# Kernel tuning notes

Hardware: AMD Instinct MI355X
Metric: run time of the kernel (lower is better)

The kernel has to match this reference:

```python
import jax, jax.numpy as jnp
import numpy as np
from jax.scipy.linalg import solve_triangular

T, DZ, DX = 4096, 64, 64


def setup_inputs() -> dict:
    key = jax.random.key(0)
    ks = jax.random.split(key, 8)
    observations = jax.random.normal(ks[0], (T, DX), jnp.float32)
    # stable transition matrix (spectral radius < 1)
    A = 0.9 * jnp.eye(DZ, dtype=jnp.float32) + (0.05 / np.sqrt(DZ)) * jax.random.normal(ks[1], (DZ, DZ), jnp.float32)
    b = 0.01 * jax.random.normal(ks[2], (DZ,), jnp.float32)
    qf = jax.random.normal(ks[3], (DZ, DZ), jnp.float32) / np.sqrt(DZ)
    Q = qf @ qf.T + 0.1 * jnp.eye(DZ, dtype=jnp.float32)  # SPD process noise
    H = jax.random.normal(ks[4], (DX, DZ), jnp.float32) / np.sqrt(DZ)
    c = 0.01 * jax.random.normal(ks[5], (DX,), jnp.float32)
    rf = jax.random.normal(ks[6], (DX, DX), jnp.float32) / np.sqrt(DX)
    R = rf @ rf.T + 0.1 * jnp.eye(DX, dtype=jnp.float32)  # SPD observation noise
    prior_mean = jnp.zeros((DZ,), jnp.float32)
    prior_cov = jnp.eye(DZ, dtype=jnp.float32)
    return dict(observations=observations, A=A, b=b, Q=Q, H=H, c=c, R=R,
                prior_mean=prior_mean, prior_cov=prior_cov)


def _update(m, P, y, H, c, R):
    # Kalman update + Gaussian log-likelihood term (stable Cholesky form of
    # the torch.inverse / MultivariateNormal math).
    yhat = H @ m + c                      # predicted obs mean
    S = H @ P @ H.T + R                   # innovation covariance [dx,dx]
    K = jnp.linalg.solve(S, H @ P).T      # gain = P H^T S^{-1} (S, P symmetric)
    r = y - yhat
    fm = m + K @ r
    fP = P - K @ H @ P
    L = jnp.linalg.cholesky(S)
    z = solve_triangular(L, r, lower=True)
    dx = y.shape[0]
    ll = (-0.5 * dx * jnp.log(2.0 * jnp.pi)
          - jnp.sum(jnp.log(jnp.diag(L)))
          - 0.5 * jnp.sum(z * z))
    return fm, fP, ll


def reference(observations, A, b, Q, H, c, R, prior_mean, prior_cov):
    # ---- filter ----
    fm0, fP0, ll0 = _update(prior_mean, prior_cov, observations[0], H, c, R)

    def fstep(carry, y):
        m, P = carry
        pm = A @ m + b                    # predict
        pP = A @ P @ A.T + Q
        fm, fP, ll = _update(pm, pP, y, H, c, R)
        return (fm, fP), (pm, pP, fm, fP, ll)

    _, (pms, pPs, fms, fPs, lls) = jax.lax.scan(fstep, (fm0, fP0), observations[1:])
    pm = jnp.concatenate([prior_mean[None], pms])   # [T, dz]
    pP = jnp.concatenate([prior_cov[None], pPs])    # [T, dz, dz]
    fm = jnp.concatenate([fm0[None], fms])
    fP = jnp.concatenate([fP0[None], fPs])
    loglikelihood = ll0 + jnp.sum(lls)

    # ---- RTS smoother (backward recursion) ----
    def bstep(carry, xs):
        sm, sP = carry
        fmt, fPt, pmn, pPn = xs
        C = jnp.linalg.solve(pPn, A @ fPt).T          # fP A^T pP^{-1}
        sm_t = fmt + C @ (sm - pmn)
        sP_t = fPt + C @ (sP - pPn) @ C.T
        return (sm_t, sP_t), (sm_t, sP_t)

    _, (sms, sPs) = jax.lax.scan(bstep, (fm[-1], fP[-1]),
                                 (fm[:-1], fP[:-1], pm[1:], pP[1:]), reverse=True)
    smoothed_means = jnp.concatenate([sms, fm[-1][None]])
    smoothed_covs = jnp.concatenate([sPs, fP[-1][None]])
    return smoothed_means, smoothed_covs, loglikelihood
```

## Files before the change

kernel.cpp:

```cpp
#include <hip/hip_runtime.h>
#include <math.h>

#define NN 64
#define LDW 68
#define LCH 32
#define N1CAP 144
#define N0MAX 144
#define EPS_HARD 1e-5f
#define EPS_GATE 5e-2f
#define STALL_WIN 5
#define STALL_IMP 0.75f

struct KP {
  const float *Y, *A, *b, *Q, *H, *c, *R, *pm0, *P0;
  float *out_mean, *out_cov, *out_ll;
  int *meta; float *metaF;
  float *fm;
  float *AT, *HT, *HA, *Hb;
  float *Fss, *Kss, *Sinvss, *Css, *CsTss, *pPss, *sPss, *Fpow, *Cpow32, *Cpow31, *uss;
  float *Pw2, *Pw4, *Pw8, *Pw16, *Pw64, *Pw128;
  float *FpwHi, *CpwHi;
  float *Dmss, *dvnss;
  float *scanF0, *scanF1, *scanB0, *scanB1;
  float *ld_pref, *u_pref;
// ... 51 lines not shown
    int base = (e>>6)*LDW + (e&63);
    *(float4*)(D + base) = *(const float4*)(S + base);
  }
  __syncthreads();
}
__device__ __forceinline__ void set_id(float* W) {
  for (int e = threadIdx.x; e < 4096; e += 256)
    W[(e>>6)*LDW + (e&63)] = ((e>>6) == (e&63)) ? 1.f : 0.f;
  __syncthreads();
}
__device__ __forceinline__ void store_id_sub(float* G, const float* W) {
  for (int e = threadIdx.x; e < 4096; e += 256)
    G[e] = (((e>>6) == (e&63)) ? 1.f : 0.f) - W[(e>>6)*LDW + (e&63)];
  __syncthreads();
}
__device__ __forceinline__ void rsub_store(float* Gd, const float* Gs, const float* W) {
  for (int e = threadIdx.x*4; e < 4096; e += 1024) {
    int base = (e>>6)*LDW + (e&63);
    F4 a, g; a.v = *(const float4*)(W + base); g.v = *(const float4*)(Gs + e);
    F4 o; o.f[0]=g.f[0]-a.f[0]; o.f[1]=g.f[1]-a.f[1]; o.f[2]=g.f[2]-a.f[2]; o.f[3]=g.f[3]-a.f[3];
    *(float4*)(Gd + e) = o.v;
  }
  __syncthreads();
}

__device__ __forceinline__ void redpair(float& ma, float& md, float* red) {
  #pragma unroll
  for (int off = 32; off; off >>= 1) {
    ma = fmaxf(ma, __shfl_xor(ma, off, 64));
    md = fmaxf(md, __shfl_xor(md, off, 64));
  }
  const int w = threadIdx.x >> 6;
  if ((threadIdx.x & 63) == 0) { red[w] = ma; red[4 + w] = md; }
  __syncthreads();
  ma = fmaxf(fmaxf(red[0], red[1]), fmaxf(red[2], red[3]));
  md = fmaxf(fmaxf(red[4], red[5]), fmaxf(red[6], red[7]));
  __syncthreads();
}

template<int TRANSA, int TRANSB, int MODE, int LDD>
__device__ __forceinline__ void mm(float* __restrict__ D,
    const float* __restrict__ A, int lda,
    const float* __restrict__ B, int ldb,
    const float* __restrict__ ADD, int ldadd)
{
  const int tid = threadIdx.x;
  const int i0 = (tid >> 4) << 2, j0 = (tid & 15) << 2;
  float acc[4][4] = {};
  for (int k0 = 0; k0 < NN; k0 += 4) {
    F4 av[4], bv[4];
    #pragma unroll
    for (int u = 0; u < 4; ++u) {
      bv[u].v = TRANSB ? *(const float4*)(B + (j0+u)*ldb + k0)
                       : *(const float4*)(B + (k0+u)*ldb + j0);
      av[u].v = TRANSA ? *(const float4*)(A + (k0+u)*lda + i0)
                       : *(const float4*)(A + (i0+u)*lda + k0);
    }
    #pragma unroll
    for (int kk = 0; kk < 4; ++kk) {
      #pragma unroll
      for (int di = 0; di < 4; ++di) {
        float a = TRANSA ? av[kk].f[di] : av[di].f[kk];
        #pragma unroll
        for (int dj = 0; dj < 4; ++dj) {
          float bb = TRANSB ? bv[dj].f[kk] : bv[kk].f[dj];
          acc[di][dj] += a * bb;
        }
      }
    }
  }
  #pragma unroll
  for (int di = 0; di < 4; ++di) {
    if (MODE == 0 && (LDD & 3) == 0) {
      F4 o;
      #pragma unroll
      for (int dj = 0; dj < 4; ++dj) o.f[dj] = acc[di][dj];
      *(float4*)(D + (i0+di)*LDD + j0) = o.v;
    } else {
      #pragma unroll
      for (int dj = 0; dj < 4; ++dj) {
        float v = acc[di][dj];
        if (MODE == 1) v = ADD[(i0+di)*ldadd + j0+dj] + v;
        if (MODE == 2) v = ADD[(i0+di)*ldadd + j0+dj] - v;
        D[(i0+di)*LDD + j0+dj] = v;
      }
    }
  }
  __syncthreads();
}

template<int TA1,int TB1,int MO1,int LD1, int TA2,int TB2,int MO2,int LD2>
__device__ __forceinline__ void mm2(
    float* __restrict__ D1, const float* __restrict__ A1, int lda1,
    const float* __restrict__ B1, int ldb1, const float* __restrict__ AD1, int ldad1,
    float* __restrict__ D2, const float* __restrict__ A2, int lda2,
    const float* __restrict__ B2, int ldb2, const float* __restrict__ AD2, int ldad2)
{
  const int tid = threadIdx.x;
  const int i0 = (tid >> 4) << 2, j0 = (tid & 15) << 2;
  float acc1[4][4] = {}, acc2[4][4] = {};
  for (int k0 = 0; k0 < NN; k0 += 4) {
    F4 av1[4], bv1[4], av2[4], bv2[4];
    #pragma unroll
    for (int u = 0; u < 4; ++u) {
      bv1[u].v = TB1 ? *(const float4*)(B1 + (j0+u)*ldb1 + k0)
                     : *(const float4*)(B1 + (k0+u)*ldb1 + j0);
      av1[u].v = TA1 ? *(const float4*)(A1 + (k0+u)*lda1 + i0)
                     : *(const float4*)(A1 + (i0+u)*lda1 + k0);
      bv2[u].v = TB2 ? *(const float4*)(B2 + (j0+u)*ldb2 + k0)
                     : *(const float4*)(B2 + (k0+u)*ldb2 + j0);
      av2[u].v = TA2 ? *(const float4*)(A2 + (k0+u)*lda2 + i0)
                     : *(const float4*)(A2 + (i0+u)*lda2 + k0);
    }
    #pragma unroll
    for (int kk = 0; kk < 4; ++kk) {
      #pragma unroll
      for (int di = 0; di < 4; ++di) {
        float a1 = TA1 ? av1[kk].f[di] : av1[di].f[kk];
        float a2 = TA2 ? av2[kk].f[di] : av2[di].f[kk];
        #pragma unroll
        for (int dj = 0; dj < 4; ++dj) {
          acc1[di][dj] += a1 * (TB1 ? bv1[dj].f[kk] : bv1[kk].f[dj]);
          acc2[di][dj] += a2 * (TB2 ? bv2[dj].f[kk] : bv2[kk].f[dj]);
        }
      }
    }
  }
  #pragma unroll
  for (int di = 0; di < 4; ++di) {
    if (MO1 == 0 && (LD1 & 3) == 0) {
      F4 o;
      #pragma unroll
      for (int dj = 0; dj < 4; ++dj) o.f[dj] = acc1[di][dj];
      *(float4*)(D1 + (i0+di)*LD1 + j0) = o.v;
    } else {
      #pragma unroll
      for (int dj = 0; dj < 4; ++dj) {
        float v = acc1[di][dj];
        if (MO1 == 1) v = AD1[(i0+di)*ldad1 + j0+dj] + v;
        if (MO1 == 2) v = AD1[(i0+di)*ldad1 + j0+dj] - v;
        D1[(i0+di)*LD1 + j0+dj] = v;
      }
    }
  }
  #pragma unroll
  for (int di = 0; di < 4; ++di) {
    if (MO2 == 0 && (LD2 & 3) == 0) {
      F4 o;
      #pragma unroll
      for (int dj = 0; dj < 4; ++dj) o.f[dj] = acc2[di][dj];
      *(float4*)(D2 + (i0+di)*LD2 + j0) = o.v;
    } else {
      #pragma unroll
      for (int dj = 0; dj < 4; ++dj) {
        float v = acc2[di][dj];
        if (MO2 == 1) v = AD2[(i0+di)*ldad2 + j0+dj] + v;
        if (MO2 == 2) v = AD2[(i0+di)*ldad2 + j0+dj] - v;
        D2[(i0+di)*LD2 + j0+dj] = v;
      }
    }
  }
  __syncthreads();
}

template<bool WANTLOG>
__device__ __forceinline__ void chol68(float* __restrict__ Sm, float* part, float* invd) {
  const int tid = threadIdx.x;
  const int lane = tid & 63;
  #pragma unroll
  for (int p = 0; p < 4; ++p) {
    const int j0 = p * 16;
    if (p > 0) {
      const int i = tid & 63;
      const int jq = (tid >> 6) * 4;
      float acc[4] = {0.f, 0.f, 0.f, 0.f};
      for (int kb = 0; kb < j0; kb += 4) {
        F4 av; av.v = *(const float4*)(Sm + i*LDW + kb);
        #pragma unroll
        for (int q = 0; q < 4; ++q) {
          F4 bv; bv.v = *(const float4*)(Sm + (j0 + jq + q)*LDW + kb);
          acc[q] += av.f[0]*bv.f[0] + av.f[1]*bv.f[1] + av.f[2]*bv.f[2] + av.f[3]*bv.f[3];
        }
      }
      #pragma unroll
      for (int q = 0; q < 4; ++q)
        Sm[i*LDW + j0 + jq + q] -= acc[q];
      __syncthreads();
    }
    if (tid < 64) {
      float t[16];
      F4 tv;
      #pragma unroll
      for (int q4 = 0; q4 < 4; ++q4) {
        tv.v = *(const float4*)(Sm + lane*LDW + j0 + 4*q4);
        t[4*q4] = tv.f[0]; t[4*q4+1] = tv.f[1]; t[4*q4+2] = tv.f[2]; t[4*q4+3] = tv.f[3];
      }
      #pragma unroll
      for (int jj = 0; jj < 16; ++jj) {
        float acc = t[jj];
        #pragma unroll
        for (int kk = 0; kk < jj; ++kk)
          acc -= __shfl(t[kk], j0 + jj, 64) * t[kk];
        float piv = __shfl(acc, j0 + jj, 64);
        float sq = sqrtf(fmaxf(piv, 1e-30f));
        float inv = 1.0f / sq;
        if (lane == j0 + jj) {
          t[jj] = sq;
          invd[j0 + jj] = inv;
          if (WANTLOG) part[j0 + jj] = logf(sq);
        } else {
          t[jj] = (lane > j0 + jj) ? acc * inv : 0.f;
        }
      }
      #pragma unroll
      for (int q4 = 0; q4 < 4; ++q4) {
        tv.f[0] = t[4*q4]; tv.f[1] = t[4*q4+1]; tv.f[2] = t[4*q4+2]; tv.f[3] = t[4*q4+3];
        *(float4*)(Sm + lane*LDW + j0 + 4*q4) = tv.v;
      }
    }
    __syncthreads();
  }
}

template<int TR>
__device__ __forceinline__ void tri_fwd_ld(const float* __restrict__ L,
                                           const float* __restrict__ invd,
                                           const float* __restrict__ SRC, int lds,
                                           float* __restrict__ DST, int ldd) {
  const int col = threadIdx.x >> 2, p = threadIdx.x & 3;
  const int gbase = (threadIdx.x & 63) & ~3;
  float xr[16];
  #pragma unroll
  for (int u = 0; u < 16; ++u)
    xr[u] = TR ? SRC[col*lds + (4*u+p)] : SRC[(4*u+p)*lds + col];
  #pragma unroll
  for (int i = 0; i < NN; ++i) {
    const int idx = i >> 2, ow = i & 3;
    float yi = xr[idx] * invd[i];
    yi = __shfl(yi, gbase + ow, 64);
    if (p == ow) xr[idx] = yi;
    else if (p > ow) xr[idx] -= L[(4*idx+p)*LDW + i] * yi;
    #pragma unroll
// ... 189 lines not shown
    if (p == ow) xr[idx] = yi;
    else if (p < ow) xr[idx] -= L[i*LDW + 4*idx+p] * yi;
    if (p == ow) xs[idx] = zi;
    else if (p < ow) xs[idx] -= L[i*LDW + 4*idx+p] * zi;
    #pragma unroll
    for (int u = 0; u < idx; ++u) {
      xr[u] -= L[i*LDW + 4*u+p] * yi;
      xs[u] -= L[i*LDW + 4*u+p] * zi;
    }
  }
  #pragma unroll
  for (int u = 0; u < 16; ++u) {
    X1[(4*u+p)*LDW + col] = xr[u];
    X2[(4*u+p)*LDW + col] = xs[u];
  }
  __syncthreads();
}

__device__ __forceinline__ void matvec2(float* __restrict__ y,
    const float* __restrict__ M1, const float* __restrict__ x1,
    const float* __restrict__ M2, const float* __restrict__ x2,
    const float* __restrict__ addv, float* __restrict__ red) {
  const int r = threadIdx.x & 63, p = threadIdx.x >> 6;
  const int kb = p*16;
  float s = 0.f;
  #pragma unroll
  for (int q = 0; q < 4; ++q) {
    F4 mv; mv.v = *(const float4*)(M1 + r*NN + kb + q*4);
    s += mv.f[0]*x1[kb+q*4] + mv.f[1]*x1[kb+q*4+1] + mv.f[2]*x1[kb+q*4+2] + mv.f[3]*x1[kb+q*4+3];
    F4 nv; nv.v = *(const float4*)(M2 + r*NN + kb + q*4);
    s += nv.f[0]*x2[kb+q*4] + nv.f[1]*x2[kb+q*4+1] + nv.f[2]*x2[kb+q*4+2] + nv.f[3]*x2[kb+q*4+3];
  }
  red[p*64 + r] = s;
  __syncthreads();
  if (threadIdx.x < 64) {
    float t = red[r] + red[64+r] + red[128+r] + red[192+r];
    y[r] = t + addv[r];
  }
  __syncthreads();
}

__device__ __forceinline__ void matvec256(float* __restrict__ y, const float* __restrict__ Mg,
    const float* __restrict__ x, const float* __restrict__ addv, float* __restrict__ red) {
  const int r = threadIdx.x & 63, p = threadIdx.x >> 6;
  const int kb = p*16;
  float s = 0.f;
  #pragma unroll
  for (int q = 0; q < 4; ++q) {
    F4 mv; mv.v = *(const float4*)(Mg + r*NN + kb + q*4);
    s += mv.f[0]*x[kb+q*4] + mv.f[1]*x[kb+q*4+1] + mv.f[2]*x[kb+q*4+2] + mv.f[3]*x[kb+q*4+3];
  }
  red[p*64 + r] = s;
  __syncthreads();
  if (threadIdx.x < 64) {
    float t = red[r] + red[64+r] + red[128+r] + red[192+r];
    y[r] = t + (addv ? addv[r] : 0.f);
  }
  __syncthreads();
}


__global__ __launch_bounds__(256) void k0(KP P) {
  __shared__ __align__(16) float W0[LDW*NN];
  const int tid = threadIdx.x;
  for (int e = tid; e < 4096; e += 256) {
    int r = e>>6, cc = e&63;
    P.AT[e] = P.A[cc*64+r];
    P.HT[e] = P.H[cc*64+r];
  }
  if (tid < 64) {
    float s = 0.f;
    for (int k = 0; k < 64; ++k) s += P.H[tid*64+k]*P.b[k];
    P.Hb[tid] = s;
  }
  __syncthreads();
  mm<0,0,0,LDW>(W0, P.H, NN, P.A, NN, nullptr, 0);
  l2g(P.HA, W0);
}

__global__ __launch_bounds__(256) void kA(KP P) {
  __shared__ __align__(16) float LA[LDW*NN], LC[LDW*NN], LJ[LDW*NN], LL[LDW*NN];
  __shared__ __align__(16) float W0[LDW*NN], W1[LDW*NN], W2[LDW*NN], W3[LDW*NN], W4[LDW*NN];
  __shared__ float part[64], iv1[64], iv2[64];
  const int tid = threadIdx.x;
  mm2<0,0,0,LDW, 0,0,0,LDW>(W0, P.H,NN, P.Q,NN, nullptr,0,
                            W2, P.H,NN, P.P0,NN, nullptr,0);
  mm2<0,1,1,LDW, 0,1,1,LDW>(W1, W0,LDW, P.H,NN, P.R,NN,
                            W3, W2,LDW, P.H,NN, P.R,NN);
  chol68<false>(W1, part, iv1);
  chol68<false>(W3, part, iv2);
  tri_fwd2<0,0>(W1, iv1, P.HA,NN, W4,LDW,
                W3, iv2, W2,LDW,  W2,LDW);
  mm2<1,0,0,LDW, 1,0,2,LDW>(LJ, W4,LDW, W4,LDW, nullptr,0,
                            W3, W2,LDW, W2,LDW, P.P0,NN);
  l2g(P.fP, W3);
  copyW(LL, LJ);
  chol68<false>(LL, part, iv2);
  tri_fb2(W1, iv1, W0,LDW, W3,LDW,  W4,LDW, W4,LDW);
  mm2<1,0,2,LDW, 1,0,2,LDW>(LA, W0,LDW, W4,LDW, P.A,NN,
                            LC, W3,LDW, W3,LDW, P.Q,NN);
  l2g3(P.EA, LA, P.EC, LC, P.EL, LL);
  for (int j = 0; j < 5 && (2 << j) <= P.N0cap - 1; ++j) {
    mm2<0,0,0,LDW, 1,0,0,LDW>(W0, LC,LDW, LL,LDW, nullptr,0,
                              W2, LL,LDW, LA,LDW, nullptr,0);
    mm<1,0,0,LDW>(W1, LL,LDW, W0,LDW, nullptr,0);
    if (tid < 64) W1[tid*LDW + tid] += 1.f;
    __syncthreads();
    chol68<false>(W1, part, iv1);
    tri_fwd2<0,1>(W1, iv1, W2,LDW, W2,LDW,
                  W1, iv1, W0,LDW, W3,LDW);
    mm2<1,0,1,LDW, 1,0,2,LDW>(LJ, W2,LDW, W2,LDW, LJ,LDW,
                              W4, W3,LDW, W3,LDW, LC,LDW);
    copyW(LL, LJ);
    chol68<false>(LL, part, iv2);
    tri_bwd_ld(W1, iv1, W2,LDW, W2,LDW);
    mm<0,0,2,LDW>(W3, W0,LDW, W2,LDW, LA,LDW);
    mm2<0,0,0,LDW, 0,0,0,LDW>(W2, LA,LDW, W3,LDW, nullptr,0,
                              W0, LA,LDW, W4,LDW, nullptr,0);
    mm<0,1,1,LDW>(LC, W0,LDW, LA,LDW, LC,LDW);
    copyW(LA, W2);
    l2g3(P.EA+(size_t)(j+1)*4096, LA, P.EC+(size_t)(j+1)*4096, LC,
         P.EL+(size_t)(j+1)*4096, LL);
  }
}

__global__ __launch_bounds__(256) void kB(KP P) {
  __shared__ __align__(16) float Wc[LDW*NN], W0[LDW*NN], W1[LDW*NN], W2[LDW*NN];
  __shared__ float part[64], ivw[64];
  const int t = blockIdx.x;
  if (t == 0) {
    for (int e = threadIdx.x*4; e < 4096; e += 1024)
      *(float4*)(P.pP + e) = *(const float4*)(P.P0 + e);
    __syncthreads();
    mm<0,0,0,LDW>(W1, P.A, NN, P.fP, NN, nullptr, 0);
    mm<0,0,1,LDW>(W0, W1, LDW, P.AT, NN, P.Q, NN);
    l2g(P.pP + 4096, W0);
    return;
  }
  g2l(Wc, P.fP);
  int rem = t;
  for (int j = 5; j >= 0; --j) {
    const int pw = 1 << j;
    if (j > 0 && pw > P.N0cap - 1) continue;
    while (rem >= pw) {
      const float* Ag = P.EA + j*4096;
      const float* Cg = P.EC + j*4096;
      const float* Lg = P.EL + j*4096;
      mm<0,0,0,LDW>(W0, Wc, LDW, Lg, NN, nullptr, 0);
      mm<1,0,0,LDW>(W1, Lg, NN, W0, LDW, nullptr, 0);
      if (threadIdx.x < 64) W1[threadIdx.x*LDW + threadIdx.x] += 1.f;
      __syncthreads();
      chol68<false>(W1, part, ivw);
      tri_fwd_ld<1>(W1, ivw, W0, LDW, W2, LDW);
      mm<1,0,2,LDW>(W1, W2, LDW, W2, LDW, Wc, LDW);
      mm<0,0,0,LDW>(W0, Ag, NN, W1, LDW, nullptr, 0);
      mm<0,1,1,LDW>(Wc, W0, LDW, Ag, NN, Cg, NN);
      rem -= pw;
    }
  }
  l2g(P.fP + (size_t)t*4096, Wc);
  mm<0,0,0,LDW>(W0, P.A, NN, Wc, LDW, nullptr, 0);
  mm<0,0,1,LDW>(W1, W0, LDW, P.AT, NN, P.Q, NN);
  l2g(P.pP + (size_t)(t+1)*4096, W1);
}

__global__ __launch_bounds__(256) void kC(KP P) {
  __shared__ float red[16];
  const int t = blockIdx.x;
  const float* cur = P.fP + (size_t)t*4096;
  const float* prv = P.fP + (size_t)(t > 0 ? t-1 : 0)*4096;
  float a = 0.f, d = 0.f;
  for (int e = threadIdx.x*4; e < 4096; e += 1024) {
    F4 v, pv; v.v = *(const float4*)(cur + e); pv.v = *(const float4*)(prv + e);
    #pragma unroll
    for (int q = 0; q < 4; ++q) {
      a = fmaxf(a, fabsf(v.f[q]));
      d = fmaxf(d, fabsf(v.f[q] - pv.f[q]));
    }
  }
  redpair(a, d, red);
  if (threadIdx.x == 0) { P.astat[t] = a; P.dstat[t] = (t > 0) ? d : 0.f; }
}

__global__ __launch_bounds__(256) void kN(KP P) {
  __shared__ float as_[N0MAX], ds_[N0MAX];
  const int cap = P.N0cap;
  for (int i = threadIdx.x; i < cap; i += 256) { as_[i] = P.astat[i]; ds_[i] = P.dstat[i]; }
  __syncthreads();
  if (threadIdx.x == 0) {
    float mabs = 1e-20f, dref = 1e30f;
    int tref = 0, N0 = cap;
    bool conv = false;
    for (int t = 0; t < cap; ++t) {
      mabs = fmaxf(mabs, as_[t]);
      if (t > 0) {
        float d = ds_[t];
        if (d <= EPS_HARD*mabs) { N0 = t+1; conv = true; }
        if (d < STALL_IMP*dref) { dref = d; tref = t; }
        else if (t - tref >= STALL_WIN && t >= 12 && d < EPS_GATE*mabs) { N0 = t+1; conv = true; }
      }
      if (conv) break;
    }
    P.meta[0] = N0; P.metaF[1] = mabs;
  }
}

__global__ __launch_bounds__(256) void k1x(KP P) {
  __shared__ __align__(16) float W0[LDW*NN], W1[LDW*NN], W2[LDW*NN], CH[LDW*NN];
  __shared__ float part[64], invd[64];
  const int tid = threadIdx.x;
  const int N0 = P.meta[0];
  if ((int)blockIdx.x == (int)gridDim.x - 1) {
    const float* fPssG = P.fP + (size_t)(N0-1)*4096;
    g2l(CH, fPssG);
    mm<0,0,0,LDW>(W1, P.A, NN, CH, LDW, nullptr, 0);
    mm<0,0,1,LDW>(W0, W1, LDW, P.AT, NN, P.Q, NN);
    l2g(P.pPss, W0);
    mm<0,0,0,LDW>(W1, P.H, NN, W0, LDW, nullptr, 0);
    mm<0,0,1,LDW>(CH, W1, LDW, P.HT, NN, P.R, NN);
    chol68<true>(CH, part, invd);
    if (tid == 0) { float s=0.f; for (int j=0;j<64;++j) s += part[j]; P.metaF[0] = s; }
    set_id(W0);
    tri_s2x2(CH, invd, W1, W0);
    l2g_T(P.Kss, W1);
    if (tid < 64) {
      float s = P.b[tid];
      for (int k = 0; k < 64; ++k) s -= W1[k*LDW + tid]*P.Hb[k];
      P.uss[tid] = s;
    }
    __syncthreads();
    l2g(P.Sinvss, W0);
    mm<1,0,2,LDW>(W0, W1, LDW, P.HA, NN, P.A, NN);
    l2g(P.Fss, W0);
    mm<0,0,0,LDW>(W1, P.A, NN, fPssG, NN, nullptr, 0);
// ... 232 lines not shown
    const int t = bid - P.NC;
    if (t >= N0) return;
    const int step = 128, sidx = 1;
    const float* Msrc = sidx ? P.scM1 : P.scM0;
    const float* Gsrc = sidx ? P.scG1 : P.scG0;
    float* Mdst = sidx ? P.scM0 : P.scM1;
    float* Gdst = sidx ? P.scG0 : P.scG1;
    const int s = t + step;
    if (s >= N0) {
      for (int e = tid*4; e < 4096; e += 1024) {
        *(float4*)(Mdst + (size_t)t*4096 + e) = *(const float4*)(Msrc + (size_t)t*4096 + e);
        *(float4*)(Gdst + (size_t)t*4096 + e) = *(const float4*)(Gsrc + (size_t)t*4096 + e);
      }
      return;
    }
    const float* Mt = Msrc + (size_t)t*4096;
    mm2<0,0,0,LDW, 0,0,0,NN>(W1, Mt,NN, Gsrc + (size_t)s*4096,NN, nullptr,0,
                             Mdst + (size_t)t*4096, Mt,NN, Msrc + (size_t)s*4096,NN, nullptr,0);
    mm<0,1,1,NN>(Gdst + (size_t)t*4096, W1, LDW, Mt, NN, Gsrc + (size_t)t*4096, NN);
  }
}

__global__ __launch_bounds__(256) void mega2(KP P) {
  __shared__ __align__(16) float W0[LDW*NN], W1[LDW*NN], W2[LDW*NN];
  __shared__ float sv[64], fmv[64], red[256];
  const int tid = threadIdx.x;
  const int bid = blockIdx.x;
  const int NC = P.NC, cap = P.N0cap, T = P.T;
  const int N0 = P.meta[0];
  const int PB = (N0 + LCH - 1)/LCH;
  if (bid < NC) {
    const int c = bid;
    if (c < PB) return;
    if (tid < 64) sv[tid] = 0.f;
    __syncthreads();
    int hi = (c == NC-1) ? T-2 : c*LCH + LCH - 1;
    for (int t = hi; t >= c*LCH; --t) {
      if (tid < 64) fmv[tid] = P.fm[(size_t)t*64+tid];
      __syncthreads();
      matvec2(sv, P.Css, sv, P.Dmss, fmv, P.dvnss, red);
    }
    if (c == NC-1) {
      if (tid < 64) fmv[tid] = P.fm[(size_t)(T-1)*64 + tid];
      __syncthreads();
      matvec256(sv, P.Cpow31, fmv, sv, red);
    }
    if (tid < 64) P.scanB0[(size_t)c*64 + tid] = sv[tid];
  } else if (bid < NC + T) {
    const int t = bid - NC;
    if (t < N0) return;
    float* dst = P.out_cov + (size_t)t*4096;
    if (t < T - N1CAP) {
      for (int e = tid*4; e < 4096; e += 1024)
        *(float4*)(dst+e) = *(const float4*)(P.sPss + e);
      return;
    }
    const int k = T - 1 - t;
    if (k == 0) {
      const float* src = P.fP + (size_t)(N0-1)*4096;
      for (int e = tid*4; e < 4096; e += 1024)
        *(float4*)(dst+e) = *(const float4*)(src+e);
      return;
    }
    const float* pw[8] = {P.Css, P.Pw2, P.Pw4, P.Pw8, P.Pw16, P.Cpow32, P.Pw64, P.Pw128};
    int b = __ffs(k) - 1;
    g2l(W1, pw[b]);
    float* cur = W1; float* oth = W0;
    for (int j = b+1; j < 8; ++j) {
      if ((k >> j) & 1) {
        mm<0,0,0,LDW>(oth, pw[j], NN, cur, LDW, nullptr, 0);
        float* tmp = cur; cur = oth; oth = tmp;
      }
    }
    mm<0,0,0,LDW>(W2, cur, LDW, P.E0g, NN, nullptr, 0);
    mm<0,1,1,LDW>(oth, W2, LDW, cur, LDW, P.sPss, NN);
    l2g(dst, oth);
  } else if (bid < NC + T + cap) {
    const int t = bid - NC - T;
    if (t >= N0) return;
    const float* Mt = P.scM0 + (size_t)t*4096;
    mm<0,0,0,LDW>(W1, Mt, NN, P.sPss, NN, nullptr, 0);
    mm<0,1,1,NN>(P.out_cov + (size_t)t*4096, W1, LDW, Mt, NN,
                 P.scG0 + (size_t)t*4096, NN);
  } else {
    const int t = bid - NC - T - cap;
    const int r = tid;
    if (t == 0) {
      if (r < 64) fmv[r] = P.pm0[r];
      __syncthreads();
    } else {
      if (r < 64) sv[r] = P.fm[(size_t)(t-1)*64 + r];
      __syncthreads();
      if (r < 64) {
        float s = P.b[r];
        const float* Ar = P.A + r*64;
        for (int k = 0; k < 64; k += 4)
          s += Ar[k]*sv[k] + Ar[k+1]*sv[k+1] + Ar[k+2]*sv[k+2] + Ar[k+3]*sv[k+3];
        fmv[r] = s;
      }
      __syncthreads();
    }
    float qq = 0.f;
    if (r < 64) {
      float rr = P.Y[(size_t)t*64 + r] - P.c[r];
      const float* Hr = P.H + r*64;
      for (int k = 0; k < 64; ++k) rr -= Hr[k]*fmv[k];
      sv[r] = rr;
    }
    __syncthreads();
    if (r < 64) {
      const float* Sv = ((t < N0) ? P.Sinvp + (size_t)t*4096 : P.Sinvss) + r*64;
      float wv = 0.f;
      for (int k = 0; k < 64; ++k) wv += Sv[k]*sv[k];
      qq = sv[r]*wv;
      #pragma unroll
      for (int off = 32; off > 0; off >>= 1) qq += __shfl_xor(qq, off, 64);
      if (r == 0) {
        float ldt = (t < N0) ? P.ld_pref[t] : P.metaF[0];
        P.llbuf[t] = -58.8120661250990555 - (double)ldt - 0.5*(double)qq;
      }
    }
  }
}

__global__ __launch_bounds__(64) void k3s(KP P, int j) {
  const int c = blockIdx.x;
  const int N0 = P.meta[0];
  const int PB = (N0 + LCH - 1)/LCH;
  if (c < PB) return;
  const int sidx = j & 1;
  const float* src = sidx ? P.scanB1 : P.scanB0;
  float* dst = sidx ? P.scanB0 : P.scanB1;
  const int off = 1 << j;
  const int r = threadIdx.x;
  float base = src[(size_t)c*64 + r];
  if (c + off <= P.NC - 1) {
    __shared__ float xv[64];
    xv[r] = src[(size_t)(c+off)*64 + r];
    __syncthreads();
    const float* M;
    if (j == 0) M = P.Cpow32;
    else if (j == 1) M = P.Pw64;
    else if (j == 2) M = P.Pw128;
    else M = P.CpwHi + (size_t)(j-3)*4096;
    const float* Mr = M + r*64;
    float s = base;
    for (int k = 0; k < 64; k += 4)
      s += Mr[k]*xv[k] + Mr[k+1]*xv[k+1] + Mr[k+2]*xv[k+2] + Mr[k+3]*xv[k+3];
    dst[(size_t)c*64 + r] = s;
  } else {
    dst[(size_t)c*64 + r] = base;
  }
}

__global__ __launch_bounds__(256) void mega3(KP P) {
  __shared__ float sv[64], fmv[64], red[256];
  __shared__ double rd[256];
  const int tid = threadIdx.x;
  const int bid = blockIdx.x;
  const int N0 = P.meta[0];
  const int PB = (N0 + LCH - 1)/LCH;
  if (bid == 0) {
    const int PE = PB*LCH;
    if (tid < 64) {
      P.out_mean[(size_t)(P.T-1)*64+tid] = P.fm[(size_t)(P.T-1)*64+tid];
      sv[tid] = P.scanB1[(size_t)PB*64 + tid];
    }
    __syncthreads();
    for (int t = PE-1; t >= 0; --t) {
      const float* Ct  = (t < N0) ? P.Cp  + (size_t)t*4096 : P.Css;
      const float* Dmt = (t < N0) ? P.Dmp + (size_t)t*4096 : P.Dmss;
      const float* dvt = (t < N0) ? P.dvnp + t*64 : P.dvnss;
      if (tid < 64) fmv[tid] = P.fm[(size_t)t*64+tid];
      __syncthreads();
      matvec2(sv, Ct, sv, Dmt, fmv, dvt, red);
      if (tid < 64) P.out_mean[(size_t)t*64+tid] = sv[tid];
      __syncthreads();
    }
  } else if (bid <= P.NC) {
    const int c = bid - 1;
    if (c < PB) return;
    if (tid < 64) {
      sv[tid] = (c == P.NC-1) ? P.fm[(size_t)(P.T-1)*64+tid]
                              : P.scanB1[(size_t)(c+1)*64 + tid];
    }
    __syncthreads();
    int hi = (c == P.NC-1) ? P.T-2 : c*LCH + LCH - 1;
    for (int t = hi; t >= c*LCH; --t) {
      if (tid < 64) fmv[tid] = P.fm[(size_t)t*64+tid];
      __syncthreads();
      matvec2(sv, P.Css, sv, P.Dmss, fmv, P.dvnss, red);
      if (tid < 64) P.out_mean[(size_t)t*64+tid] = sv[tid];
      __syncthreads();
    }
  } else {
    double s = 0.0;
    for (int t = tid; t < P.T; t += 256) s += P.llbuf[t];
    rd[tid] = s; __syncthreads();
    #pragma unroll
    for (int off = 128; off > 0; off >>= 1) {
      if (tid < off) rd[tid] += rd[tid + off];
      __syncthreads();
    }
    if (tid == 0) P.out_ll[0] = (float)rd[0];
  }
}


extern "C" void kernel_launch(void* const* d_in, const int* in_sizes, int n_in,
                              void* d_out, int out_size, void* d_ws, size_t ws_size,
                              hipStream_t stream) {
  (void)n_in; (void)out_size;
  KP P;
  P.Y   = (const float*)d_in[0];
  P.A   = (const float*)d_in[1];
  P.b   = (const float*)d_in[2];
  P.Q   = (const float*)d_in[3];
  P.H   = (const float*)d_in[4];
  P.c   = (const float*)d_in[5];
  P.R   = (const float*)d_in[6];
  P.pm0 = (const float*)d_in[7];
  P.P0  = (const float*)d_in[8];
  const int T = in_sizes[0] / 64;
  const int NC = T / LCH;
  P.T = T; P.NC = NC;

  float* out = (float*)d_out;
  P.out_mean = out;
  P.out_cov  = out + (size_t)T*64;
  P.out_ll   = out + (size_t)T*64 + (size_t)T*4096;

  float* w = (float*)d_ws;
  size_t off = 0;
  auto alloc = [&](size_t n) { float* p = w + off; off += n; return p; };
  P.meta   = (int*)alloc(8);
  P.metaF  = alloc(8);
  P.llbuf  = (double*)alloc((size_t)2*T);
  P.fm     = alloc((size_t)T*64);
  P.AT = alloc(4096); P.HT = alloc(4096); P.HA = alloc(4096); P.Hb = alloc(64);
  P.Fss = alloc(4096); P.Kss = alloc(4096); P.Sinvss = alloc(4096);
  P.Css = alloc(4096); P.CsTss = alloc(4096); P.pPss = alloc(4096); P.sPss = alloc(4096);
  P.Fpow = alloc(4096); P.Cpow32 = alloc(4096); P.Cpow31 = alloc(4096); P.uss = alloc(64);
  P.Pw2 = alloc(4096); P.Pw4 = alloc(4096); P.Pw8 = alloc(4096); P.Pw16 = alloc(4096);
  P.Pw64 = alloc(4096); P.Pw128 = alloc(4096);
  P.FpwHi = alloc((size_t)6*4096); P.CpwHi = alloc((size_t)4*4096);
  P.Dmss = alloc(4096); P.dvnss = alloc(64);
  P.scanF0 = alloc((size_t)(NC+1)*64); P.scanF1 = alloc((size_t)(NC+1)*64);
  P.scanB0 = alloc((size_t)NC*64); P.scanB1 = alloc((size_t)NC*64);
  P.E0g = alloc(4096);
  P.EA = alloc((size_t)8*4096); P.EC = alloc((size_t)8*4096);
  P.EJ = alloc((size_t)8*4096); P.EL = alloc((size_t)8*4096);
  P.astat = alloc(256); P.dstat = alloc(256);
  size_t fixed = off;
  size_t per_t = 12*4096 + 128 + 1;
  size_t total_f = ws_size / 4;
  long long avail = (long long)total_f - (long long)fixed - 4096 - 64;
  int cap = (avail > 0) ? (int)(avail / (long long)per_t) : 8;
  if (cap > N0MAX) cap = N0MAX;
  if (cap < 8) cap = 8;
  P.N0cap = cap;
  P.ld_pref = alloc(cap);
  P.u_pref  = alloc((size_t)cap*64);
  P.dvnp    = alloc((size_t)cap*64);
  P.fP    = alloc((size_t)cap*4096);
  P.pP    = alloc((size_t)(cap+1)*4096);
  P.Kp    = alloc((size_t)cap*4096);
  P.Sinvp = alloc((size_t)cap*4096);
  P.Fp    = alloc((size_t)cap*4096);
  P.Cp    = alloc((size_t)cap*4096);
  P.CsTp  = alloc((size_t)cap*4096);
  P.Dmp   = alloc((size_t)cap*4096);
  P.scM0  = alloc((size_t)cap*4096);
  P.scM1  = alloc((size_t)cap*4096);
  P.scG0  = alloc((size_t)cap*4096);
  P.scG1  = alloc((size_t)cap*4096);

  k0<<<1, 256, 0, stream>>>(P);
  kA<<<1, 256, 0, stream>>>(P);
  kB<<<cap, 256, 0, stream>>>(P);
  kC<<<cap, 256, 0, stream>>>(P);
  kN<<<1, 256, 0, stream>>>(P);
  k1x<<<cap+1, 256, 0, stream>>>(P);
  mega0<<<3 + NC + cap, 256, 0, stream>>>(P);
  for (int d = 0; d < 7; ++d)
    megaL<<<cap + NC, 256, 0, stream>>>(P, d);
  megaL7<<<NC + cap, 256, 0, stream>>>(P);
  mega2<<<NC + T + cap + T, 256, 0, stream>>>(P);
  for (int j = 0; j < 7; ++j)
    k3s<<<NC, 64, 0, stream>>>(P, j);
  mega3<<<NC + 2, 256, 0, stream>>>(P);
}
```

Baseline: 1.511 ms.

## Parallelize prefix smoother mean recursion via affine-map doubling scan

Replaces the single-block serial backward loop over the pre-steady-state prefix of smoothed means with a parallel log-depth scan over affine maps (matrix products plus vectors), run in new mega3s launches alongside the existing chunk-carry scan. This removes a long serial chain of matvecs in one block, at the cost of extra 64x64 matrix multiplies, more workspace and an additional launch. Also fuses the identity-add into the mm epilogue and removes copyW by writing dual outputs and swapping pointers in kA.

```diff
diff --git a/kernel.cpp b/kernel.cpp
--- a/kernel.cpp
+++ b/kernel.cpp
@@ -157,6 +157,7 @@
         float v = acc[di][dj];
         if (MODE == 1) v = ADD[(i0+di)*ldadd + j0+dj] + v;
         if (MODE == 2) v = ADD[(i0+di)*ldadd + j0+dj] - v;
+        if (MODE == 3) v = v + (((i0+di) == (j0+dj)) ? 1.f : 0.f);
         D[(i0+di)*LDD + j0+dj] = v;
       }
     }
@@ -233,6 +234,54 @@
         if (MO2 == 2) v = AD2[(i0+di)*ldad2 + j0+dj] - v;
         D2[(i0+di)*LD2 + j0+dj] = v;
       }
+    }
+  }
+  __syncthreads();
+}
+
+template<int MO1>
+__device__ __forceinline__ void mm2j(
+    float* __restrict__ D1, float* __restrict__ D1b,
+    const float* __restrict__ A1, const float* __restrict__ AD1,
+    float* __restrict__ D2, const float* __restrict__ A2,
+    const float* __restrict__ AD2, int ldad2)
+{
+  const int tid = threadIdx.x;
+  const int i0 = (tid >> 4) << 2, j0 = (tid & 15) << 2;
+  float acc1[4][4] = {}, acc2[4][4] = {};
+  for (int k0 = 0; k0 < NN; k0 += 4) {
+    F4 av1[4], bv1[4], av2[4], bv2[4];
+    #pragma unroll
+    for (int u = 0; u < 4; ++u) {
+      bv1[u].v = *(const float4*)(A1 + (k0+u)*LDW + j0);
+      av1[u].v = *(const float4*)(A1 + (k0+u)*LDW + i0);
+      bv2[u].v = *(const float4*)(A2 + (k0+u)*LDW + j0);
+      av2[u].v = *(const float4*)(A2 + (k0+u)*LDW + i0);
+    }
+    #pragma unroll
+    for (int kk = 0; kk < 4; ++kk) {
+      #pragma unroll
+      for (int di = 0; di < 4; ++di) {
+        float a1 = av1[kk].f[di];
+        float a2 = av2[kk].f[di];
+        #pragma unroll
+        for (int dj = 0; dj < 4; ++dj) {
+          acc1[di][dj] += a1 * bv1[kk].f[dj];
+          acc2[di][dj] += a2 * bv2[kk].f[dj];
+        }
+      }
+    }
+  }
+  #pragma unroll
+  for (int di = 0; di < 4; ++di) {
+    #pragma unroll
+    for (int dj = 0; dj < 4; ++dj) {
+      float v = acc1[di][dj];
+      if (MO1 == 1) v = AD1[(i0+di)*LDW + j0+dj] + v;
+      D1[(i0+di)*LDW + j0+dj] = v;
+      D1b[(i0+di)*LDW + j0+dj] = v;
+      float w = AD2[(i0+di)*ldad2 + j0+dj] - acc2[di][dj];
+      D2[(i0+di)*LDW + j0+dj] = w;
     }
   }
   __syncthreads();
@@ -588,45 +637,40 @@
   __shared__ __align__(16) float LA[LDW*NN], LC[LDW*NN], LJ[LDW*NN], LL[LDW*NN];
   __shared__ __align__(16) float W0[LDW*NN], W1[LDW*NN], W2[LDW*NN], W3[LDW*NN], W4[LDW*NN];
   __shared__ float part[64], iv1[64], iv2[64];
-  const int tid = threadIdx.x;
-  mm2<0,0,0,LDW, 0,0,0,LDW>(W0, P.H,NN, P.Q,NN, nullptr,0,
-                            W2, P.H,NN, P.P0,NN, nullptr,0);
-  mm2<0,1,1,LDW, 0,1,1,LDW>(W1, W0,LDW, P.H,NN, P.R,NN,
-                            W3, W2,LDW, P.H,NN, P.R,NN);
-  chol68<false>(W1, part, iv1);
-  chol68<false>(W3, part, iv2);
-  tri_fwd2<0,0>(W1, iv1, P.HA,NN, W4,LDW,
-                W3, iv2, W2,LDW,  W2,LDW);
-  mm2<1,0,0,LDW, 1,0,2,LDW>(LJ, W4,LDW, W4,LDW, nullptr,0,
-                            W3, W2,LDW, W2,LDW, P.P0,NN);
-  l2g(P.fP, W3);
-  copyW(LL, LJ);
-  chol68<false>(LL, part, iv2);
-  tri_fb2(W1, iv1, W0,LDW, W3,LDW,  W4,LDW, W4,LDW);
-  mm2<1,0,2,LDW, 1,0,2,LDW>(LA, W0,LDW, W4,LDW, P.A,NN,
-                            LC, W3,LDW, W3,LDW, P.Q,NN);
-  l2g3(P.EA, LA, P.EC, LC, P.EL, LL);
+  float *pA = LA, *pC = LC, *pJ = LJ, *pL = LL;
+  float *s0 = W0, *s1 = W1, *s2 = W2, *s3 = W3, *s4 = W4;
+  mm2<0,0,0,LDW, 0,0,0,LDW>(s0, P.H,NN, P.Q,NN, nullptr,0,
+                            s2, P.H,NN, P.P0,NN, nullptr,0);
+  mm2<0,1,1,LDW, 0,1,1,LDW>(s1, s0,LDW, P.H,NN, P.R,NN,
+                            s3, s2,LDW, P.H,NN, P.R,NN);
+  chol68<false>(s1, part, iv1);
+  chol68<false>(s3, part, iv2);
+  tri_fwd2<0,0>(s1, iv1, P.HA,NN, s4,LDW,
+                s3, iv2, s2,LDW,  s2,LDW);
+  mm2j<0>(pJ, pL, s4, nullptr, s3, s2, P.P0, NN);
+  l2g(P.fP, s3);
+  chol68<false>(pL, part, iv2);
+  tri_fb2(s1, iv1, s0,LDW, s3,LDW,  s4,LDW, s4,LDW);
+  mm2<1,0,2,LDW, 1,0,2,LDW>(pA, s0,LDW, s4,LDW, P.A,NN,
+                            pC, s3,LDW, s3,LDW, P.Q,NN);
+  l2g3(P.EA, pA, P.EC, pC, P.EL, pL);
   for (int j = 0; j < 5 && (2 << j) <= P.N0cap - 1; ++j) {
-    mm2<0,0,0,LDW, 1,0,0,LDW>(W0, LC,LDW, LL,LDW, nullptr,0,
-                              W2, LL,LDW, LA,LDW, nullptr,0);
-    mm<1,0,0,LDW>(W1, LL,LDW, W0,LDW, nullptr,0);
-    if (tid < 64) W1[tid*LDW + tid] += 1.f;
-    __syncthreads();
-    chol68<false>(W1, part, iv1);
-    tri_fwd2<0,1>(W1, iv1, W2,LDW, W2,LDW,
-                  W1, iv1, W0,LDW, W3,LDW);
-    mm2<1,0,1,LDW, 1,0,2,LDW>(LJ, W2,LDW, W2,LDW, LJ,LDW,
-                              W4, W3,LDW, W3,LDW, LC,LDW);
-    copyW(LL, LJ);
-    chol68<false>(LL, part, iv2);
-    tri_bwd_ld(W1, iv1, W2,LDW, W2,LDW);
-    mm<0,0,2,LDW>(W3, W0,LDW, W2,LDW, LA,LDW);
-    mm2<0,0,0,LDW, 0,0,0,LDW>(W2, LA,LDW, W3,LDW, nullptr,0,
-                              W0, LA,LDW, W4,LDW, nullptr,0);
-    mm<0,1,1,LDW>(LC, W0,LDW, LA,LDW, LC,LDW);
-    copyW(LA, W2);
-    l2g3(P.EA+(size_t)(j+1)*4096, LA, P.EC+(size_t)(j+1)*4096, LC,
-         P.EL+(size_t)(j+1)*4096, LL);
+    mm2<0,0,0,LDW, 1,0,0,LDW>(s0, pC,LDW, pL,LDW, nullptr,0,
+                              s2, pL,LDW, pA,LDW, nullptr,0);
+    mm<1,0,3,LDW>(s1, pL,LDW, s0,LDW, nullptr,0);
+    chol68<false>(s1, part, iv1);
+    tri_fwd2<0,1>(s1, iv1, s2,LDW, s2,LDW,
+                  s1, iv1, s0,LDW, s3,LDW);
+    mm2j<1>(pJ, pL, s2, pJ, s4, s3, pC, LDW);
+    chol68<false>(pL, part, iv2);
+    tri_bwd_ld(s1, iv1, s2,LDW, s2,LDW);
+    mm<0,0,2,LDW>(s3, s0,LDW, s2,LDW, pA,LDW);
+    mm2<0,0,0,LDW, 0,0,0,LDW>(s2, pA,LDW, s3,LDW, nullptr,0,
+                              s0, pA,LDW, s4,LDW, nullptr,0);
+    mm<0,1,1,LDW>(pC, s0,LDW, pA,LDW, pC,LDW);
+    { float* tmp = pA; pA = s2; s2 = tmp; }
+    l2g3(P.EA+(size_t)(j+1)*4096, pA, P.EC+(size_t)(j+1)*4096, pC,
+         P.EL+(size_t)(j+1)*4096, pL);
   }
 }
 
@@ -653,9 +697,7 @@
       const float* Cg = P.EC + j*4096;
       const float* Lg = P.EL + j*4096;
       mm<0,0,0,LDW>(W0, Wc, LDW, Lg, NN, nullptr, 0);
-      mm<1,0,0,LDW>(W1, Lg, NN, W0, LDW, nullptr, 0);
-      if (threadIdx.x < 64) W1[threadIdx.x*LDW + threadIdx.x] += 1.f;
-      __syncthreads();
+      mm<1,0,3,LDW>(W1, Lg, NN, W0, LDW, nullptr, 0);
       chol68<false>(W1, part, ivw);
       tri_fwd_ld<1>(W1, ivw, W0, LDW, W2, LDW);
       mm<1,0,2,LDW>(W1, W2, LDW, W2, LDW, Wc, LDW);
@@ -1054,7 +1096,7 @@
     mm<0,0,0,LDW>(W1, Mt, NN, P.sPss, NN, nullptr, 0);
     mm<0,1,1,NN>(P.out_cov + (size_t)t*4096, W1, LDW, Mt, NN,
                  P.scG0 + (size_t)t*4096, NN);
-  } else {
+  } else if (bid < NC + T + cap + T) {
     const int t = bid - NC - T - cap;
     const int r = tid;
     if (t == 0) {
@@ -1072,7 +1114,6 @@
       }
       __syncthreads();
     }
-    float qq = 0.f;
     if (r < 64) {
       float rr = P.Y[(size_t)t*64 + r] - P.c[r];
       const float* Hr = P.H + r*64;
@@ -1084,7 +1125,7 @@
       const float* Sv = ((t < N0) ? P.Sinvp + (size_t)t*4096 : P.Sinvss) + r*64;
       float wv = 0.f;
       for (int k = 0; k < 64; ++k) wv += Sv[k]*sv[k];
-      qq = sv[r]*wv;
+      float qq = sv[r]*wv;
       #pragma unroll
       for (int off = 32; off > 0; off >>= 1) qq += __shfl_xor(qq, off, 64);
       if (r == 0) {
@@ -1092,36 +1133,71 @@
         P.llbuf[t] = -58.8120661250990555 - (double)ldt - 0.5*(double)qq;
       }
     }
-  }
-}
-
-__global__ __launch_bounds__(64) void k3s(KP P, int j) {
-  const int c = blockIdx.x;
+  } else {
+    const int t = bid - NC - T - cap - T;
+    const int PE = PB*LCH;
+    if (t >= PE) return;
+    const float* Ct  = (t < N0) ? P.Cp  + (size_t)t*4096 : P.Css;
+    const float* Dmt = (t < N0) ? P.Dmp + (size_t)t*4096 : P.Dmss;
+    const float* dvt = (t < N0) ? P.dvnp + t*64 : P.dvnss;
+    for (int e = tid*4; e < 4096; e += 1024)
+      *(float4*)(P.scM1 + (size_t)t*4096 + e) = *(const float4*)(Ct + e);
+    matvec256(P.scG1 + (size_t)t*4096, Dmt, P.fm + (size_t)t*64, dvt, red);
+  }
+}
+
+__global__ __launch_bounds__(256) void mega3s(KP P, int d) {
+  __shared__ float xv[64], red[256];
+  const int tid = threadIdx.x;
+  const int bid = blockIdx.x;
   const int N0 = P.meta[0];
   const int PB = (N0 + LCH - 1)/LCH;
-  if (c < PB) return;
-  const int sidx = j & 1;
-  const float* src = sidx ? P.scanB1 : P.scanB0;
-  float* dst = sidx ? P.scanB0 : P.scanB1;
-  const int off = 1 << j;
-  const int r = threadIdx.x;
-  float base = src[(size_t)c*64 + r];
-  if (c + off <= P.NC - 1) {
-    __shared__ float xv[64];
-    xv[r] = src[(size_t)(c+off)*64 + r];
-    __syncthreads();
-    const float* M;
-    if (j == 0) M = P.Cpow32;
-    else if (j == 1) M = P.Pw64;
-    else if (j == 2) M = P.Pw128;
-    else M = P.CpwHi + (size_t)(j-3)*4096;
-    const float* Mr = M + r*64;
-    float s = base;
-    for (int k = 0; k < 64; k += 4)
-      s += Mr[k]*xv[k] + Mr[k+1]*xv[k+1] + Mr[k+2]*xv[k+2] + Mr[k+3]*xv[k+3];
-    dst[(size_t)c*64 + r] = s;
+  const int PE = PB*LCH;
+  const int PEcap = ((P.N0cap + 31)/32)*32;
+  if (bid < PEcap) {
+    const int t = bid;
+    if (t >= PE) return;
+    const float* Msrc = (d % 2 == 0) ? P.scM1 : P.scM0;
+    const float* Vsrc = (d % 2 == 0) ? P.scG1 : P.scG0;
+    float* Mdst = (d % 2 == 0) ? P.scM0 : P.scM1;
+    float* Vdst = (d % 2 == 0) ? P.scG0 : P.scG1;
+    const int s = t + (1 << d);
+    if (s >= PE) {
+      for (int e = tid*4; e < 4096; e += 1024)
+        *(float4*)(Mdst + (size_t)t*4096 + e) = *(const float4*)(Msrc + (size_t)t*4096 + e);
+      if (tid < 64) Vdst[(size_t)t*4096 + tid] = Vsrc[(size_t)t*4096 + tid];
+      return;
+    }
+    mm<0,0,0,NN>(Mdst + (size_t)t*4096, Msrc + (size_t)t*4096, NN,
+                 Msrc + (size_t)s*4096, NN, nullptr, 0);
+    matvec256(Vdst + (size_t)t*4096, Msrc + (size_t)t*4096,
+              Vsrc + (size_t)s*4096, Vsrc + (size_t)t*4096, red);
   } else {
-    dst[(size_t)c*64 + r] = base;
+    if (d >= 7) return;
+    const int c = bid - PEcap;
+    if (c < PB || c >= P.NC) return;
+    const int sidx = d & 1;
+    const float* src = sidx ? P.scanB1 : P.scanB0;
+    float* dst = sidx ? P.scanB0 : P.scanB1;
+    const int off = 1 << d;
+    if (c + off <= P.NC - 1) {
+      if (tid < 64) xv[tid] = src[(size_t)(c+off)*64 + tid];
+      __syncthreads();
+      if (tid < 64) {
+        const float* M;
+        if (d == 0) M = P.Cpow32;
+        else if (d == 1) M = P.Pw64;
+        else if (d == 2) M = P.Pw128;
+        else M = P.CpwHi + (size_t)(d-3)*4096;
+        const float* Mr = M + tid*64;
+        float s = src[(size_t)c*64 + tid];
+        for (int k = 0; k < 64; k += 4)
+          s += Mr[k]*xv[k] + Mr[k+1]*xv[k+1] + Mr[k+2]*xv[k+2] + Mr[k+3]*xv[k+3];
+        dst[(size_t)c*64 + tid] = s;
+      }
+    } else {
+      if (tid < 64) dst[(size_t)c*64 + tid] = src[(size_t)c*64 + tid];
+    }
   }
 }
 
@@ -1132,25 +1208,9 @@
   const int bid = blockIdx.x;
   const int N0 = P.meta[0];
   const int PB = (N0 + LCH - 1)/LCH;
-  if (bid == 0) {
-    const int PE = PB*LCH;
-    if (tid < 64) {
-      P.out_mean[(size_t)(P.T-1)*64+tid] = P.fm[(size_t)(P.T-1)*64+tid];
-      sv[tid] = P.scanB1[(size_t)PB*64 + tid];
-    }
-    __syncthreads();
-    for (int t = PE-1; t >= 0; --t) {
-      const float* Ct  = (t < N0) ? P.Cp  + (size_t)t*4096 : P.Css;
-      const float* Dmt = (t < N0) ? P.Dmp + (size_t)t*4096 : P.Dmss;
-      const float* dvt = (t < N0) ? P.dvnp + t*64 : P.dvnss;
-      if (tid < 64) fmv[tid] = P.fm[(size_t)t*64+tid];
-      __syncthreads();
-      matvec2(sv, Ct, sv, Dmt, fmv, dvt, red);
-      if (tid < 64) P.out_mean[(size_t)t*64+tid] = sv[tid];
-      __syncthreads();
-    }
-  } else if (bid <= P.NC) {
-    const int c = bid - 1;
+  const int PEcap = ((P.N0cap + 31)/32)*32;
+  if (bid < P.NC) {
+    const int c = bid;
     if (c < PB) return;
     if (tid < 64) {
       sv[tid] = (c == P.NC-1) ? P.fm[(size_t)(P.T-1)*64+tid]
@@ -1165,6 +1225,16 @@
       if (tid < 64) P.out_mean[(size_t)t*64+tid] = sv[tid];
       __syncthreads();
     }
+  } else if (bid < P.NC + PEcap) {
+    const int t = bid - P.NC;
+    const int PE = PB*LCH;
+    if (t == 0) {
+      if (tid < 64) P.out_mean[(size_t)(P.T-1)*64+tid] = P.fm[(size_t)(P.T-1)*64+tid];
+      __syncthreads();
+    }
+    if (t >= PE) return;
+    matvec256(P.out_mean + (size_t)t*64, P.scM1 + (size_t)t*4096,
+              P.scanB1 + (size_t)PB*64, P.scG1 + (size_t)t*4096, red);
   } else {
     double s = 0.0;
     for (int t = tid; t < P.T; t += 256) s += P.llbuf[t];
@@ -1226,11 +1296,13 @@
   size_t fixed = off;
   size_t per_t = 12*4096 + 128 + 1;
   size_t total_f = ws_size / 4;
-  long long avail = (long long)total_f - (long long)fixed - 4096 - 64;
+  long long avail = (long long)total_f - (long long)fixed - 4096 - 64
+                  - 4LL*32*4096;
   int cap = (avail > 0) ? (int)(avail / (long long)per_t) : 8;
   if (cap > N0MAX) cap = N0MAX;
   if (cap < 8) cap = 8;
   P.N0cap = cap;
+  const int PEcap = ((cap + 31)/32)*32;
   P.ld_pref = alloc(cap);
   P.u_pref  = alloc((size_t)cap*64);
   P.dvnp    = alloc((size_t)cap*64);
@@ -1242,10 +1314,10 @@
   P.Cp    = alloc((size_t)cap*4096);
   P.CsTp  = alloc((size_t)cap*4096);
   P.Dmp   = alloc((size_t)cap*4096);
-  P.scM0  = alloc((size_t)cap*4096);
-  P.scM1  = alloc((size_t)cap*4096);
-  P.scG0  = alloc((size_t)cap*4096);
-  P.scG1  = alloc((size_t)cap*4096);
+  P.scM0  = alloc((size_t)(cap+32)*4096);
+  P.scM1  = alloc((size_t)(cap+32)*4096);
+  P.scG0  = alloc((size_t)(cap+32)*4096);
+  P.scG1  = alloc((size_t)(cap+32)*4096);
 
   k0<<<1, 256, 0, stream>>>(P);
   kA<<<1, 256, 0, stream>>>(P);
@@ -1257,8 +1329,8 @@
   for (int d = 0; d < 7; ++d)
     megaL<<<cap + NC, 256, 0, stream>>>(P, d);
   megaL7<<<NC + cap, 256, 0, stream>>>(P);
-  mega2<<<NC + T + cap + T, 256, 0, stream>>>(P);
-  for (int j = 0; j < 7; ++j)
-    k3s<<<NC, 64, 0, stream>>>(P, j);
-  mega3<<<NC + 2, 256, 0, stream>>>(P);
-}
+  mega2<<<NC + T + cap + T + PEcap, 256, 0, stream>>>(P);
+  for (int d = 0; d < 8; ++d)
+    mega3s<<<PEcap + NC, 256, 0, stream>>>(P, d);
+  mega3<<<NC + PEcap + 1, 256, 0, stream>>>(P);
+}
```

Result: no change. 1.515 ms (+0.3%).
